# Optimization experiments

Measured on AMD Instinct MI355X. Metric: run time of the kernel, lower is better.

Reference implementation:

```python
import jax, jax.numpy as jnp
import numpy as np

N_NODES = 100000
N_EDGES = 600000
D_IN = 128
HID = 128
N_LAYERS = 3


def gcn_conv(x, W, b, src, dst, num_nodes):
    """PyG-style GCNConv: D^{-1/2}(A+I)D^{-1/2} X W + b (self-loops added)."""
    h = x @ W  # [N, H]
    # in-degree including self-loop
    deg = jnp.zeros((num_nodes,), dtype=x.dtype).at[dst].add(1.0) + 1.0
    dinv = jax.lax.rsqrt(deg)
    norm = dinv[src] * dinv[dst]  # [E]
    msg = h[src] * norm[:, None]  # [E, H] gather + scale
    out = jax.ops.segment_sum(msg, dst, num_segments=num_nodes)  # scatter-add
    out = out + h * (1.0 / deg)[:, None]  # self-loop term (norm = 1/deg)
    return out + b


def setup_inputs() -> dict:
    key = jax.random.key(0)
    ks = jax.random.split(key, 16)
    x = jax.random.normal(ks[0], (N_NODES, D_IN), dtype=jnp.float32)
    edge_index = jax.random.randint(ks[1], (2, N_EDGES), 0, N_NODES, dtype=jnp.int64)
    timestamp = jax.random.uniform(ks[2], (1,), dtype=jnp.float32)
    # GCN layer weights (glorot-ish scale) and biases
    def glorot(k, fan_in, fan_out):
        s = jnp.sqrt(6.0 / (fan_in + fan_out))
        return jax.random.uniform(k, (fan_in, fan_out), minval=-s, maxval=s, dtype=jnp.float32)
    W_gcn = [glorot(ks[3], D_IN, HID), glorot(ks[4], HID, HID), glorot(ks[5], HID, HID)]
    b_gcn = [jnp.zeros((HID,), jnp.float32) for _ in range(N_LAYERS)]
    # temporal gate MLP: Linear(1,H) -> tanh -> Linear(H,H) -> sigmoid
    Wg1 = glorot(ks[6], 1, HID)
    bg1 = jnp.zeros((HID,), jnp.float32)
    Wg2 = glorot(ks[7], HID, HID)
    bg2 = jnp.zeros((HID,), jnp.float32)
    return {
        "x": x, "edge_index": edge_index, "timestamp": timestamp,
        "W0": W_gcn[0], "b0": b_gcn[0],
        "W1": W_gcn[1], "b1": b_gcn[1],
        "W2": W_gcn[2], "b2": b_gcn[2],
        "Wg1": Wg1, "bg1": bg1, "Wg2": Wg2, "bg2": bg2,
    }


def reference(x, edge_index, timestamp, W0, b0, W1, b1, W2, b2, Wg1, bg1, Wg2, bg2):
    src, dst = edge_index[0], edge_index[1]
    num_nodes = x.shape[0]
    # temporal gate: [1,1] -> [1,H], broadcast over nodes
    t = timestamp.reshape(1, 1)
    gate = jax.nn.sigmoid(jnp.tanh(t @ Wg1 + bg1) @ Wg2 + bg2)  # [1, H]
    for (W, b) in ((W0, b0), (W1, b1), (W2, b2)):
        x = gcn_conv(x, W, b, src, dst, num_nodes)
        x = jax.nn.relu(x)
        x = x * gate  # broadcast gate over nodes
        # dropout: identity in eval mode
    return x
```

## Files before the change

kernel.cpp:

```cpp
#include <hip/hip_runtime.h>
#include <hip/hip_bf16.h>
#include <hip/hip_fp16.h>
#include <math.h>


#define D 128

typedef __attribute__((ext_vector_type(8))) short short8;
typedef __attribute__((ext_vector_type(8))) _Float16 half8;
typedef __attribute__((ext_vector_type(4))) float floatx4;

__device__ __forceinline__ unsigned bf16_rne(float x) {
    unsigned u = __float_as_uint(x);
    return (u + 0x7FFFu + ((u >> 16) & 1u)) >> 16;
}

__device__ __forceinline__ void gload_lds16(const void* g, void* l) {
    __builtin_amdgcn_global_load_lds(
        (const __attribute__((address_space(1))) unsigned int*)g,
        (__attribute__((address_space(3))) unsigned int*)l, 16, 0, 0);
}

__device__ __forceinline__ float h2f(unsigned short u) {
    return __half2float(__ushort_as_half(u));
}

__global__ __launch_bounds__(256) void prep_kernel(
    const int* __restrict__ w, int* __restrict__ src32,
    int* __restrict__ dst32, int* __restrict__ counts, int E,
    const float* __restrict__ W0, const float* __restrict__ W1,
    const float* __restrict__ W2, short8* __restrict__ Wf_hi,
    short8* __restrict__ Wf_lo,
    const float* __restrict__ t, const float* __restrict__ Wg1,
    const float* __restrict__ bg1, const float* __restrict__ Wg2,
    const float* __restrict__ bg2, float* __restrict__ gate)
{
    int b = blockIdx.x;
    if (b < 24) {
        int f = b * 256 + threadIdx.x;
        int layer = f >> 11;
        int fi = f & 2047;
        int lane = fi & 63;
        int tt = fi >> 6;
        int kc = tt >> 3, n = tt & 7;
        const float* W = (layer == 0) ? W0 : (layer == 1) ? W1 : W2;
        int krow = kc * 32 + (lane >> 4) * 8;
        int col = n * 16 + (lane & 15);
        short8 hv, lv;
        if (layer == 0) {
            #pragma unroll
            for (int j = 0; j < 8; j++) {
                float x = W[(size_t)(krow + j) * D + col];
                unsigned hb = bf16_rne(x);
                float hf = __uint_as_float(hb << 16);
                unsigned lb = bf16_rne(x - hf);
                hv[j] = (short)hb;
                lv[j] = (short)lb;
            }
        } else {
            #pragma unroll
            for (int j = 0; j < 8; j++) {
                float x = W[(size_t)(krow + j) * D + col];
                __half hh = __float2half(x);
                float hf = __half2float(hh);
                __half ll = __float2half(x - hf);
                hv[j] = (short)__half_as_ushort(hh);
                lv[j] = (short)__half_as_ushort(ll);
            }
        }
        Wf_hi[f] = hv;
        Wf_lo[f] = lv;
        return;
    }
    if (b == 24) {
        __shared__ float u[D];
        int j = threadIdx.x;
        if (j < D) {
            float tv = t[0];
            u[j] = tanhf(tv * Wg1[j] + bg1[j]);
        }
        __syncthreads();
        if (j < D) {
            float s = bg2[j];
            #pragma unroll 8
            for (int k = 0; k < D; k++) s += u[k] * Wg2[k * D + j];
            gate[j] = 1.0f / (1.0f + expf(-s));
        }
        return;
    }
    __shared__ int flag;
    if (threadIdx.x == 0) {
        int z = 0;
        for (int k = 0; k < 64; k++) z |= w[2 * k + 1];
        flag = (z == 0) ? 1 : 0;
    }
    __syncthreads();
    int i64 = flag;
    int e = (b - 25) * 256 + threadIdx.x;
    if (e >= E) return;
    int s = i64 ? w[2 * e] : w[e];
    int d = i64 ? w[2 * (E + e)] : w[E + e];
    src32[e] = s;
    dst32[e] = d;
    atomicAdd(&counts[d], 1);
}

#define SCHUNK 1024
__device__ __forceinline__ int cap4(int c) { return (c + 3) & ~3; }

__global__ __launch_bounds__(256) void scan_partial_kernel(
    const int* __restrict__ counts, int* __restrict__ bsums, int N)
{
    int base = blockIdx.x * SCHUNK + threadIdx.x * 4;
    int s = 0;
    if (base + 3 < N) {
        int4 v = *(const int4*)(counts + base);
        s = cap4(v.x) + cap4(v.y) + cap4(v.z) + cap4(v.w);
    } else {
        for (int k = 0; k < 4; k++) if (base + k < N) s += cap4(counts[base + k]);
    }
    #pragma unroll
    for (int off = 1; off < 64; off <<= 1) s += __shfl_xor(s, off);
    __shared__ int wsum[4];
    int lane = threadIdx.x & 63, wid = threadIdx.x >> 6;
    if (lane == 0) wsum[wid] = s;
    __syncthreads();
    if (threadIdx.x == 0)
        bsums[blockIdx.x] = wsum[0] + wsum[1] + wsum[2] + wsum[3];
}

__global__ __launch_bounds__(1024) void scan_bsums_kernel(
    int* __restrict__ bsums, int* __restrict__ total_out, int B)
{
    int t = threadIdx.x;
    int v = (t < B) ? bsums[t] : 0;
    int lane = t & 63, wid = t >> 6;
    int s = v;
    #pragma unroll
    for (int off = 1; off < 64; off <<= 1) {
        int n = __shfl_up(s, off);
        if (lane >= off) s += n;
    }
    __shared__ int wsum[16], wpre[16];
    if (lane == 63) wsum[wid] = s;
    __syncthreads();
    if (t < 16) {
        int ws = wsum[t];
        #pragma unroll
        for (int off = 1; off < 16; off <<= 1) {
            int n = __shfl_up(ws, off);
            if (t >= off) ws += n;
        }
        wpre[t] = ws;
    }
    __syncthreads();
    int wex = wid ? wpre[wid - 1] : 0;
    if (t < B) bsums[t] = wex + (s - v);
    if (t == 0) *total_out = wpre[15];
}

__global__ __launch_bounds__(256) void scan_final_kernel(
    const int* __restrict__ counts, const int* __restrict__ bsums,
    int* __restrict__ offsets, int* __restrict__ cursor,
    float* __restrict__ dinv, int N)
{
    int base = blockIdx.x * SCHUNK + threadIdx.x * 4;
    int c[4];
    float dd[4];
    bool full = (base + 3 < N);
    if (full) {
        int4 v = *(const int4*)(counts + base);
        c[0] = cap4(v.x); c[1] = cap4(v.y); c[2] = cap4(v.z); c[3] = cap4(v.w);
        dd[0] = rsqrtf((float)(v.x + 1)); dd[1] = rsqrtf((float)(v.y + 1));
        dd[2] = rsqrtf((float)(v.z + 1)); dd[3] = rsqrtf((float)(v.w + 1));
    } else {
        for (int k = 0; k < 4; k++) {
            int r = (base + k < N) ? counts[base + k] : 0;
            c[k] = (base + k < N) ? cap4(r) : 0;
            dd[k] = rsqrtf((float)(r + 1));
        }
    }
    int sum = c[0] + c[1] + c[2] + c[3];
    int lane = threadIdx.x & 63, wid = threadIdx.x >> 6;
    int s = sum;
    #pragma unroll
    for (int off = 1; off < 64; off <<= 1) {
        int n = __shfl_up(s, off);
        if (lane >= off) s += n;
    }
    __shared__ int wsum[4], wpre[4];
    if (lane == 63) wsum[wid] = s;
    __syncthreads();
    if (threadIdx.x == 0) {
        int a = 0;
        #pragma unroll
        for (int k = 0; k < 4; k++) { wpre[k] = a; a += wsum[k]; }
    }
    __syncthreads();
    int e0 = bsums[blockIdx.x] + wpre[wid] + (s - sum);
    int4 o = make_int4(e0, e0 + c[0], e0 + c[0] + c[1], e0 + c[0] + c[1] + c[2]);
    float4 dv = make_float4(dd[0], dd[1], dd[2], dd[3]);
    if (full) {
        *(int4*)(offsets + base) = o;
        *(int4*)(cursor + base) = o;
        *(float4*)(dinv + base) = dv;
    } else {
        int oo[4] = { o.x, o.y, o.z, o.w };
        for (int k = 0; k < 4; k++)
            if (base + k < N) {
                offsets[base + k] = oo[k];
                cursor[base + k] = oo[k];
                dinv[base + k] = dd[k];
            }
    }
}

__global__ __launch_bounds__(256) void bucket_kernel(
    const int* __restrict__ src32, const int* __restrict__ dst32,
    const float* __restrict__ dinv, int* __restrict__ cursor,
    int2* __restrict__ edges8, int E)
{
    int e = blockIdx.x * blockDim.x + threadIdx.x;
    if (e >= E) return;
    int s = src32[e];
    int d = dst32[e];
    float f = dinv[s];
    int pos = atomicAdd(&cursor[d], 1);
    edges8[pos] = make_int2(s, __float_as_int(f));
}

#define WSTAGE(kc_)                                                           \
    {                                                                         \
        short* wb_ = Wfs + (((kc_) & 1) ? 8192 : 0);                          \
        const short8* gh_ = Wf_hi + (size_t)(kc_) * 512;                      \
        const short8* gl_ = Wf_lo + (size_t)(kc_) * 512;                      \
        _Pragma("unroll")                                                     \
        for (int i_ = 0; i_ < 2; i_++) {                                      \
            int c_ = i_ * 256 + w * 64;                                       \
            gload_lds16(gh_ + c_ + lane, wb_ + c_ * 8);                       \
            gload_lds16(gl_ + c_ + lane, wb_ + 4096 + c_ * 8);                \
        }                                                                     \
    }

#define MFMA_BLOCK(kc)                                                        \
    {                                                                         \
        const short* wb = Wfs + (((kc) & 1) ? 8192 : 0);                      \
        _Pragma("unroll")                                                     \
        for (int n = 0; n < 8; n++) {                                         \
            short8 bh = *(const short8*)(wb + (n * 64 + lane) * 8);           \
            short8 bl = *(const short8*)(wb + 4096 + (n * 64 + lane) * 8);    \
            acc[0][n] = __builtin_amdgcn_mfma_f32_16x16x32_bf16(ah0, bh, acc[0][n], 0, 0, 0); \
            acc[0][n] = __builtin_amdgcn_mfma_f32_16x16x32_bf16(ah0, bl, acc[0][n], 0, 0, 0); \
            acc[0][n] = __builtin_amdgcn_mfma_f32_16x16x32_bf16(al0, bh, acc[0][n], 0, 0, 0); \
            acc[1][n] = __builtin_amdgcn_mfma_f32_16x16x32_bf16(ah1, bh, acc[1][n], 0, 0, 0); \
            acc[1][n] = __builtin_amdgcn_mfma_f32_16x16x32_bf16(ah1, bl, acc[1][n], 0, 0, 0); \
            acc[1][n] = __builtin_amdgcn_mfma_f32_16x16x32_bf16(al1, bh, acc[1][n], 0, 0, 0); \
        }                                                                     \
    }

#define MFMA_BLOCK_F16(kc)                                                    \
    {                                                                         \
        const short* wb = Wfs + (((kc) & 1) ? 8192 : 0);                      \
        _Pragma("unroll")                                                     \
        for (int n = 0; n < 8; n++) {                                         \
            half8 bh = *(const half8*)(wb + (n * 64 + lane) * 8);             \
            half8 bl = *(const half8*)(wb + 4096 + (n * 64 + lane) * 8);      \
            acc[0][n] = __builtin_amdgcn_mfma_f32_16x16x32_f16(ah0, bh, acc[0][n], 0, 0, 0); \
            acc[0][n] = __builtin_amdgcn_mfma_f32_16x16x32_f16(ah0, bl, acc[0][n], 0, 0, 0); \
            acc[1][n] = __builtin_amdgcn_mfma_f32_16x16x32_f16(ah1, bh, acc[1][n], 0, 0, 0); \
            acc[1][n] = __builtin_amdgcn_mfma_f32_16x16x32_f16(ah1, bl, acc[1][n], 0, 0, 0); \
        }                                                                     \
    }

#define EPILOGUE()                                                            \
    _Pragma("unroll")                                                         \
    for (int rt = 0; rt < 2; rt++) {                                          \
        _Pragma("unroll")                                                     \
        for (int reg = 0; reg < 4; reg++) {                                   \
            int row = rowbase + rt * 16 + qd * 4 + reg;                       \
            if (row < M) {                                                    \
                unsigned short* hp = H16 + (size_t)row * D + m16;             \
                _Pragma("unroll")                                             \
                for (int n = 0; n < 8; n++)                                   \
                    hp[n * 16] = __half_as_ushort(__float2half(acc[rt][n][reg])); \
            }                                                                 \
        }                                                                     \
    }

#define GBM 128
__device__ __forceinline__ void cvt8(const float* f, short8& hi, short8& lo) {
    #pragma unroll
    for (int j = 0; j < 8; j++) {
        unsigned hb = bf16_rne(f[j]);
        float hf = __uint_as_float(hb << 16);
        unsigned lb = bf16_rne(f[j] - hf);
        hi[j] = (short)hb;
        lo[j] = (short)lb;
    }
}

__global__ __launch_bounds__(256) void gemm_f32_kernel(
    const float* __restrict__ X, const short8* __restrict__ Wf_hi,
    const short8* __restrict__ Wf_lo, unsigned short* __restrict__ H16, int M)
{
    __shared__ short Wfs[16384];
    int tid = threadIdx.x;
    int w = tid >> 6, lane = tid & 63;
    int m16 = lane & 15, qd = lane >> 4;
    int rowbase = blockIdx.x * GBM + w * 32;

    int r0 = rowbase + m16;      if (r0 >= M) r0 = M - 1;
    int r1 = rowbase + m16 + 16; if (r1 >= M) r1 = M - 1;
    const float* xp0 = X + (size_t)r0 * D + qd * 8;
    const float* xp1 = X + (size_t)r1 * D + qd * 8;

    floatx4 acc[2][8];
    #pragma unroll
    for (int rt = 0; rt < 2; rt++)
        #pragma unroll
        for (int n = 0; n < 8; n++)
            acc[rt][n] = (floatx4)(0.f);

    #define LOADA(kc_, A0, A1)                                              \
        {                                                                   \
            *(float4*)(A0)     = *(const float4*)(xp0 + (kc_) * 32);        \
            *(float4*)(A0 + 4) = *(const float4*)(xp0 + (kc_) * 32 + 4);    \
            *(float4*)(A1)     = *(const float4*)(xp1 + (kc_) * 32);        \
            *(float4*)(A1 + 4) = *(const float4*)(xp1 + (kc_) * 32 + 4);    \
        }

    float a0c[8], a1c[8], a0n[8], a1n[8];
    WSTAGE(0)
    LOADA(0, a0c, a1c)

    #pragma unroll
    for (int kc = 0; kc < 4; kc++) {
        __syncthreads();
        if (kc < 3) {
            WSTAGE(kc + 1)
            LOADA(kc + 1, a0n, a1n)
        }
        short8 ah0, al0, ah1, al1;
        cvt8(a0c, ah0, al0);
        cvt8(a1c, ah1, al1);
        MFMA_BLOCK(kc)
        if (kc < 3) {
            #pragma unroll
            for (int z = 0; z < 8; z++) { a0c[z] = a0n[z]; a1c[z] = a1n[z]; }
        }
    }
    #undef LOADA
    EPILOGUE()
}

__global__ __launch_bounds__(256) void gemm_f16_kernel(
    const unsigned short* __restrict__ Xh,
    const short8* __restrict__ Wf_hi, const short8* __restrict__ Wf_lo,
    unsigned short* __restrict__ H16, int M)
{
    __shared__ short Wfs[16384];
    int tid = threadIdx.x;
    int w = tid >> 6, lane = tid & 63;
    int m16 = lane & 15, qd = lane >> 4;
    int rowbase = blockIdx.x * GBM + w * 32;

    int r0 = rowbase + m16;      if (r0 >= M) r0 = M - 1;
    int r1 = rowbase + m16 + 16; if (r1 >= M) r1 = M - 1;
    const unsigned short* xh0 = Xh + (size_t)r0 * D + qd * 8;
    const unsigned short* xh1 = Xh + (size_t)r1 * D + qd * 8;

    floatx4 acc[2][8];
    #pragma unroll
    for (int rt = 0; rt < 2; rt++)
        #pragma unroll
        for (int n = 0; n < 8; n++)
            acc[rt][n] = (floatx4)(0.f);

    half8 ah0, ah1, nh0, nh1;
    WSTAGE(0)
    ah0 = *(const half8*)(xh0);
    ah1 = *(const half8*)(xh1);

    #pragma unroll
    for (int kc = 0; kc < 4; kc++) {
        __syncthreads();
        if (kc < 3) {
            WSTAGE(kc + 1)
            nh0 = *(const half8*)(xh0 + (kc + 1) * 32);
            nh1 = *(const half8*)(xh1 + (kc + 1) * 32);
        }
        MFMA_BLOCK_F16(kc)
        if (kc < 3) { ah0 = nh0; ah1 = nh1; }
    }
    EPILOGUE()
}

__global__ __launch_bounds__(256) void agg_kernel(
    const unsigned short* __restrict__ H16, const int2* __restrict__ edges,
    const int* __restrict__ offsets, const float* __restrict__ dinv,
    const float* __restrict__ bias, const float* __restrict__ gate,
    float* __restrict__ outF, unsigned short* __restrict__ outH,
    int M, int writeF32)
{
    int t = threadIdx.x;
    int hw = t >> 5;
    int l32 = t & 31;
    int node = blockIdx.x * 8 + hw;
    if (node >= M) return;

    int beg = offsets[node];
    int end = offsets[node + 1];
    float dv = dinv[node];
    const unsigned short* __restrict__ Hc = H16 + l32 * 4;
    ushort4 us = *(const ushort4*)(Hc + (size_t)node * D);
    float4 acc = make_float4(0.f, 0.f, 0.f, 0.f);

    if (beg < end) {
        int4 p0 = *(const int4*)(edges + beg);
        int4 p1 = *(const int4*)(edges + beg + 2);
        ushort4 u0 = *(const ushort4*)(Hc + (size_t)p0.x * D);
        ushort4 u1 = *(const ushort4*)(Hc + (size_t)p0.z * D);
        ushort4 u2 = *(const ushort4*)(Hc + (size_t)p1.x * D);
        ushort4 u3 = *(const ushort4*)(Hc + (size_t)p1.z * D);
        int j1 = (beg + 4 < end) ? beg + 4 : beg;
        int4 q0 = *(const int4*)(edges + j1);
        int4 q1 = *(const int4*)(edges + j1 + 2);

        for (int j = beg; j < end; j += 4) {
            int jn = j + 8;
            int jp = (jn < end) ? jn : beg;
            int4 r0 = *(const int4*)(edges + jp);
            int4 r1 = *(const int4*)(edges + jp + 2);
            ushort4 v0 = *(const ushort4*)(Hc + (size_t)q0.x * D);
            ushort4 v1 = *(const ushort4*)(Hc + (size_t)q0.z * D);
            ushort4 v2 = *(const ushort4*)(Hc + (size_t)q1.x * D);
            ushort4 v3 = *(const ushort4*)(Hc + (size_t)q1.z * D);
            float n0 = __int_as_float(p0.y) * dv, n1 = __int_as_float(p0.w) * dv;
            float n2 = __int_as_float(p1.y) * dv, n3 = __int_as_float(p1.w) * dv;
            acc.x = fmaf(h2f(u3.x), n3, fmaf(h2f(u2.x), n2, fmaf(h2f(u1.x), n1, fmaf(h2f(u0.x), n0, acc.x))));
            acc.y = fmaf(h2f(u3.y), n3, fmaf(h2f(u2.y), n2, fmaf(h2f(u1.y), n1, fmaf(h2f(u0.y), n0, acc.y))));
            acc.z = fmaf(h2f(u3.z), n3, fmaf(h2f(u2.z), n2, fmaf(h2f(u1.z), n1, fmaf(h2f(u0.z), n0, acc.z))));
            acc.w = fmaf(h2f(u3.w), n3, fmaf(h2f(u2.w), n2, fmaf(h2f(u1.w), n1, fmaf(h2f(u0.w), n0, acc.w))));
            p0 = q0; p1 = q1; q0 = r0; q1 = r1;
            u0 = v0; u1 = v1; u2 = v2; u3 = v3;
        }
    }

    float nself = dv * dv;
    acc.x = fmaf(h2f(us.x), nself, acc.x);
    acc.y = fmaf(h2f(us.y), nself, acc.y);
    acc.z = fmaf(h2f(us.z), nself, acc.z);
    acc.w = fmaf(h2f(us.w), nself, acc.w);

    float4 bv = *(const float4*)(bias + l32 * 4);
    float4 gv = *(const float4*)(gate + l32 * 4);
    acc.x = fmaxf(acc.x + bv.x, 0.f) * gv.x;
    acc.y = fmaxf(acc.y + bv.y, 0.f) * gv.y;
    acc.z = fmaxf(acc.z + bv.z, 0.f) * gv.z;
    acc.w = fmaxf(acc.w + bv.w, 0.f) * gv.w;

    if (writeF32) {
        *(float4*)(outF + (size_t)node * D + l32 * 4) = acc;
    } else {
        ushort4 hs = make_ushort4(
            __half_as_ushort(__float2half(acc.x)),
            __half_as_ushort(__float2half(acc.y)),
            __half_as_ushort(__float2half(acc.z)),
            __half_as_ushort(__float2half(acc.w)));
        *(ushort4*)(outH + (size_t)node * D + l32 * 4) = hs;
    }
}

static inline size_t align_up(size_t v, size_t a) { return (v + a - 1) & ~(a - 1); }

extern "C" void kernel_launch(void* const* d_in, const int* in_sizes, int n_in,
                              void* d_out, int out_size, void* d_ws, size_t ws_size,
                              hipStream_t stream)
{
    const float* x   = (const float*)d_in[0];
    const int*   ei  = (const int*)d_in[1];
    const float* ts  = (const float*)d_in[2];
    const float* Wl[3] = { (const float*)d_in[3], (const float*)d_in[5], (const float*)d_in[7] };
    const float* bl[3] = { (const float*)d_in[4], (const float*)d_in[6], (const float*)d_in[8] };
    const float* Wg1 = (const float*)d_in[9];
    const float* bg1 = (const float*)d_in[10];
    const float* Wg2 = (const float*)d_in[11];
    const float* bg2 = (const float*)d_in[12];

    const int N = in_sizes[0] / D;
    const int E = in_sizes[1] / 2;
    const int NB = (N + SCHUNK - 1) / SCHUNK;
    const size_t ECAP = (size_t)E + 3 * (size_t)N;

    char* p = (char*)d_ws;
    unsigned short* h16 = (unsigned short*)p; p += align_up((size_t)N * D * 2, 256);
    unsigned short* xh  = (unsigned short*)p; p += align_up((size_t)N * D * 2, 256);
    int* src32  = (int*)p;   p += align_up((size_t)E * 4, 256);
    int* dst32  = (int*)p;   p += align_up((size_t)E * 4, 256);
    int* counts = (int*)p;   p += align_up((size_t)N * 4, 256);
    float* dinv = (float*)p; p += align_up((size_t)N * 4, 256);
    int* offs   = (int*)p;   p += align_up((size_t)(N + 1) * 4, 256);
    int* cursor = (int*)p;   p += align_up((size_t)N * 4, 256);
    int2* edges8 = (int2*)p; p += align_up(ECAP * 8, 256);
    float* gate = (float*)p; p += align_up((size_t)D * 4, 256);
    int* bsums  = (int*)p;   p += align_up((size_t)NB * 4, 256);
    short8* Wf_hi = (short8*)p; p += align_up((size_t)3 * 2048 * 16, 256);
    short8* Wf_lo = (short8*)p; p += align_up((size_t)3 * 2048 * 16, 256);
    (void)ws_size; (void)n_in; (void)out_size;

    (void)hipMemsetAsync(counts, 0, (size_t)N * 4, stream);
    (void)hipMemsetAsync(edges8, 0, ECAP * 8, stream);

    int egrid = (E + 255) / 256;
    prep_kernel<<<25 + egrid, 256, 0, stream>>>(
        ei, src32, dst32, counts, E,
        Wl[0], Wl[1], Wl[2], Wf_hi, Wf_lo,
        ts, Wg1, bg1, Wg2, bg2, gate);
    scan_partial_kernel<<<NB, 256, 0, stream>>>(counts, bsums, N);
    scan_bsums_kernel<<<1, 1024, 0, stream>>>(bsums, offs + N, NB);
    scan_final_kernel<<<NB, 256, 0, stream>>>(counts, bsums, offs, cursor, dinv, N);
    bucket_kernel<<<egrid, 256, 0, stream>>>(src32, dst32, dinv, cursor, edges8, E);

    int ggrid = (N + GBM - 1) / GBM;
    int agrid = (N + 7) / 8;
    gemm_f32_kernel<<<ggrid, 256, 0, stream>>>(x, Wf_hi, Wf_lo, h16, N);
    agg_kernel<<<agrid, 256, 0, stream>>>(h16, edges8, offs, dinv, bl[0], gate,
                                          nullptr, xh, N, 0);
    gemm_f16_kernel<<<ggrid, 256, 0, stream>>>(xh, Wf_hi + 2048, Wf_lo + 2048, h16, N);
    agg_kernel<<<agrid, 256, 0, stream>>>(h16, edges8, offs, dinv, bl[1], gate,
                                          nullptr, xh, N, 0);
    gemm_f16_kernel<<<ggrid, 256, 0, stream>>>(xh, Wf_hi + 4096, Wf_lo + 4096, h16, N);
    agg_kernel<<<agrid, 256, 0, stream>>>(h16, edges8, offs, dinv, bl[2], gate,
                                          (float*)d_out, nullptr, N, 1);
}
```

Before: 237.5 us.

## Replace per-edge global atomic bucketing with two-pass binned CSR placement

Replaces the single bucket kernel, which did one global atomic per edge on a per-node cursor and scattered writes randomly, with two passes. The first bins edges into coarse 256-node regions using LDS counters and one global atomic per region per block. The second places each region's edges into CSR order in LDS and writes them out coalesced, including zero padding. This drops the full memset of the edge buffer and adds an extra staging buffer and a second read and write of the edges.

```diff
diff --git a/kernel.cpp b/kernel.cpp
--- a/kernel.cpp
+++ b/kernel.cpp
@@ -106,6 +106,8 @@
 }
 
 #define SCHUNK 1024
+#define RBITS 8
+#define RSZ 256
 __device__ __forceinline__ int cap4(int c) { return (c + 3) & ~3; }
 
 __global__ __launch_bounds__(256) void scan_partial_kernel(
@@ -161,7 +163,7 @@
 
 __global__ __launch_bounds__(256) void scan_final_kernel(
     const int* __restrict__ counts, const int* __restrict__ bsums,
-    int* __restrict__ offsets, int* __restrict__ cursor,
+    int* __restrict__ offsets, int* __restrict__ cursor2,
     float* __restrict__ dinv, int N)
 {
     int base = blockIdx.x * SCHUNK + threadIdx.x * 4;
@@ -202,31 +204,94 @@
     float4 dv = make_float4(dd[0], dd[1], dd[2], dd[3]);
     if (full) {
         *(int4*)(offsets + base) = o;
-        *(int4*)(cursor + base) = o;
         *(float4*)(dinv + base) = dv;
     } else {
         int oo[4] = { o.x, o.y, o.z, o.w };
         for (int k = 0; k < 4; k++)
             if (base + k < N) {
                 offsets[base + k] = oo[k];
-                cursor[base + k] = oo[k];
                 dinv[base + k] = dd[k];
             }
     }
-}
-
-__global__ __launch_bounds__(256) void bucket_kernel(
+    if ((base & (RSZ - 1)) == 0 && base < N) cursor2[base >> RBITS] = e0;
+}
+
+#define P1E 16
+__global__ __launch_bounds__(256) void binpass_kernel(
     const int* __restrict__ src32, const int* __restrict__ dst32,
-    const float* __restrict__ dinv, int* __restrict__ cursor,
-    int2* __restrict__ edges8, int E)
-{
-    int e = blockIdx.x * blockDim.x + threadIdx.x;
-    if (e >= E) return;
-    int s = src32[e];
-    int d = dst32[e];
-    float f = dinv[s];
-    int pos = atomicAdd(&cursor[d], 1);
-    edges8[pos] = make_int2(s, __float_as_int(f));
+    int* __restrict__ cursor2, int2* __restrict__ stag, int E, int B)
+{
+    __shared__ int cnt[512];
+    __shared__ int base[512];
+    int tid = threadIdx.x;
+    for (int i = tid; i < B; i += 256) cnt[i] = 0;
+    __syncthreads();
+    int e0 = blockIdx.x * (P1E * 256) + tid;
+    int s[P1E], d[P1E], lp[P1E];
+    #pragma unroll
+    for (int k = 0; k < P1E; k++) {
+        int e = e0 + k * 256;
+        if (e < E) {
+            s[k] = src32[e];
+            d[k] = dst32[e];
+            lp[k] = atomicAdd(&cnt[d[k] >> RBITS], 1);
+        }
+    }
+    __syncthreads();
+    for (int i = tid; i < B; i += 256)
+        base[i] = cnt[i] ? atomicAdd(&cursor2[i], cnt[i]) : 0;
+    __syncthreads();
+    #pragma unroll
+    for (int k = 0; k < P1E; k++) {
+        int e = e0 + k * 256;
+        if (e < E)
+            stag[base[d[k] >> RBITS] + lp[k]] = make_int2(s[k], d[k]);
+    }
+}
+
+#define P2CAP 4096
+__global__ __launch_bounds__(256) void place_kernel(
+    const int2* __restrict__ stag, const int* __restrict__ cursor2,
+    const int* __restrict__ offsets, const float* __restrict__ dinv,
+    int2* __restrict__ edges8, int N)
+{
+    __shared__ int2 buf[P2CAP];
+    __shared__ int loff[RSZ + 1];
+    __shared__ int lcnt[RSZ];
+    int b = blockIdx.x;
+    int tid = threadIdx.x;
+    int d0 = b * RSZ;
+    int d1 = (d0 + RSZ < N) ? d0 + RSZ : N;
+    int nd = d1 - d0;
+    for (int i = tid; i <= nd; i += 256) loff[i] = offsets[d0 + i];
+    for (int i = tid; i < nd; i += 256) lcnt[i] = 0;
+    __syncthreads();
+    int regionStart = loff[0];
+    int regionSize = loff[nd] - regionStart;
+    int ecount = cursor2[b] - regionStart;
+    if (regionSize <= P2CAP) {
+        for (int i = tid; i < regionSize; i += 256) buf[i] = make_int2(0, 0);
+        __syncthreads();
+        for (int i = tid; i < ecount; i += 256) {
+            int2 sd = stag[regionStart + i];
+            int ld = sd.y - d0;
+            int pos = loff[ld] - regionStart + atomicAdd(&lcnt[ld], 1);
+            buf[pos] = make_int2(sd.x, __float_as_int(dinv[sd.x]));
+        }
+        __syncthreads();
+        for (int i = tid; i < regionSize; i += 256)
+            edges8[regionStart + i] = buf[i];
+    } else {
+        for (int i = tid; i < regionSize; i += 256)
+            edges8[regionStart + i] = make_int2(0, 0);
+        __syncthreads();
+        for (int i = tid; i < ecount; i += 256) {
+            int2 sd = stag[regionStart + i];
+            int ld = sd.y - d0;
+            int pos = loff[ld] + atomicAdd(&lcnt[ld], 1);
+            edges8[pos] = make_int2(sd.x, __float_as_int(dinv[sd.x]));
+        }
+    }
 }
 
 #define WSTAGE(kc_)                                                           \
@@ -490,6 +555,7 @@
     const int N = in_sizes[0] / D;
     const int E = in_sizes[1] / 2;
     const int NB = (N + SCHUNK - 1) / SCHUNK;
+    const int B  = (N + RSZ - 1) / RSZ;
     const size_t ECAP = (size_t)E + 3 * (size_t)N;
 
     char* p = (char*)d_ws;
@@ -500,7 +566,8 @@
     int* counts = (int*)p;   p += align_up((size_t)N * 4, 256);
     float* dinv = (float*)p; p += align_up((size_t)N * 4, 256);
     int* offs   = (int*)p;   p += align_up((size_t)(N + 1) * 4, 256);
-    int* cursor = (int*)p;   p += align_up((size_t)N * 4, 256);
+    int* cursor2 = (int*)p;  p += align_up((size_t)B * 4, 256);
+    int2* stag  = (int2*)p;  p += align_up(ECAP * 8, 256);
     int2* edges8 = (int2*)p; p += align_up(ECAP * 8, 256);
     float* gate = (float*)p; p += align_up((size_t)D * 4, 256);
     int* bsums  = (int*)p;   p += align_up((size_t)NB * 4, 256);
@@ -509,7 +576,6 @@
     (void)ws_size; (void)n_in; (void)out_size;
 
     (void)hipMemsetAsync(counts, 0, (size_t)N * 4, stream);
-    (void)hipMemsetAsync(edges8, 0, ECAP * 8, stream);
 
     int egrid = (E + 255) / 256;
     prep_kernel<<<25 + egrid, 256, 0, stream>>>(
@@ -518,8 +584,10 @@
         ts, Wg1, bg1, Wg2, bg2, gate);
     scan_partial_kernel<<<NB, 256, 0, stream>>>(counts, bsums, N);
     scan_bsums_kernel<<<1, 1024, 0, stream>>>(bsums, offs + N, NB);
-    scan_final_kernel<<<NB, 256, 0, stream>>>(counts, bsums, offs, cursor, dinv, N);
-    bucket_kernel<<<egrid, 256, 0, stream>>>(src32, dst32, dinv, cursor, edges8, E);
+    scan_final_kernel<<<NB, 256, 0, stream>>>(counts, bsums, offs, cursor2, dinv, N);
+    int g1 = (E + P1E * 256 - 1) / (P1E * 256);
+    binpass_kernel<<<g1, 256, 0, stream>>>(src32, dst32, cursor2, stag, E, B);
+    place_kernel<<<B, 256, 0, stream>>>(stag, cursor2, offs, dinv, edges8, N);
 
     int ggrid = (N + GBM - 1) / GBM;
     int agrid = (N + 7) / 8;
```

After: 226.9 us. 1.05x faster.
